# Kernel optimization log

Hardware: AMD Instinct MI355X
Metric: run time of the kernel (lower is better)

The kernel has to match this reference:

```python
import jax, jax.numpy as jnp
import numpy as np
from jax import lax


def _conv1d_t(x, w, pad):
    # x: [b, c, t], w: [o, c, k] -> [b, o, t]
    return lax.conv_general_dilated(x, w, (1,), ((pad, pad),),
                                    dimension_numbers=('NCH', 'OIH', 'NCH'))


def _ln_c(x, g, b, eps=1e-6):
    # LayerNorm over channel axis (axis=1) of [b, c, t] (channels_first)
    mu = x.mean(1, keepdims=True)
    var = ((x - mu) ** 2).mean(1, keepdims=True)
    return (x - mu) / jnp.sqrt(var + eps) * g[None, :, None] + b[None, :, None]


def _qgelu(x):
    return x * jax.nn.sigmoid(1.702 * x)


def _bn3d(x, g, b, eps=1e-5):
    # BatchNorm3d forward with batch statistics (training mode), x: [b, c, t, h, w]
    mu = x.mean((0, 2, 3, 4), keepdims=True)
    var = ((x - mu) ** 2).mean((0, 2, 3, 4), keepdims=True)
    return (x - mu) / jnp.sqrt(var + eps) * g[None, :, None, None, None] + b[None, :, None, None, None]


def setup_inputs() -> dict:
    key = jax.random.key(0)
    ks = jax.random.split(key, 8)
    B, C, T, H, Wd = 8, 256, 8, 56, 56
    CR = 64  # C // rf_r
    return {
        'feat': jax.random.normal(ks[0], (B, C, T, H, Wd), jnp.float32),
        'W': jax.random.normal(ks[1], (C, C, 3, 3), jnp.float32) * 0.02,
        'bias_p': jnp.zeros((C,), jnp.float32),
        'a_w': jax.random.normal(ks[2], (CR, C, 3), jnp.float32) * 0.02,
        'a_b': jnp.zeros((CR,), jnp.float32),
        'norm_w': jnp.ones((CR,), jnp.float32),
        'norm_b': jnp.zeros((CR,), jnp.float32),
        'normt_w': jnp.ones((CR,), jnp.float32),
        'normt_b': jnp.zeros((CR,), jnp.float32),
        'qkv_w': jax.random.normal(ks[3], (3 * CR, CR), jnp.float32) * 0.02,
        'qkv_b': jnp.zeros((3 * CR,), jnp.float32),
        'ao_w': jax.random.normal(ks[4], (CR, CR), jnp.float32) * 0.02,
        'ao_b': jnp.zeros((CR,), jnp.float32),
        'b_w': jax.random.normal(ks[5], (C, CR, 3), jnp.float32) * 0.02,
        'bb_w': jax.random.normal(ks[6], (C, CR, 3), jnp.float32) * 0.02,
        'gamma_a': jnp.ones((C,), jnp.float32),
        'beta_a': jnp.zeros((C,), jnp.float32),
        'gamma_b': jnp.zeros((C,), jnp.float32),
        'beta_b': jnp.zeros((C,), jnp.float32),
    }


HEAD_DIM = 64


def reference(feat, W, bias_p, a_w, a_b, norm_w, norm_b, normt_w, normt_b,
              qkv_w, qkv_b, ao_w, ao_b, b_w, bb_w,
              gamma_a, beta_a, gamma_b, beta_b):
    b, c_in, t, h, w = feat.shape
    c_out = W.shape[0]

    # ---- routing function (RouteFuncwTransformer) ----
    x = feat.mean((3, 4))                              # spatial avgpool -> [b, c, t]
    x = _conv1d_t(x, a_w, 1) + a_b[None, :, None]      # conv 'a' (kernel 3 over t)
    x = _ln_c(x, norm_w, norm_b)
    x = _qgelu(x)

    # temporal self-attention on 1x1-spatial tokens
    xn = _ln_c(x, normt_w, normt_b)
    c_r = xn.shape[1]
    nh = c_r // HEAD_DIM
    qkv = jnp.einsum('oc,bct->bot', qkv_w, xn) + qkv_b[None, :, None]
    qkv = qkv.reshape(b, 3, HEAD_DIM, nh, t)           # matches torch view(b,3,hd,nh,t)
    q = jnp.transpose(qkv[:, 0], (0, 2, 3, 1))         # [b, nh, t, hd]
    k = jnp.transpose(qkv[:, 1], (0, 2, 3, 1))
    v = jnp.transpose(qkv[:, 2], (0, 2, 3, 1))
    scale = c_r ** (-0.5)
    attn = jax.nn.softmax(jnp.einsum('bnqd,bnkd->bnqk', q, k) * scale, axis=-1)
    o = jnp.einsum('bnqk,bnkd->bnqd', attn, v)         # [b, nh, t, hd]
    o = jnp.transpose(o, (0, 1, 3, 2)).reshape(b, c_r, t)
    o = jnp.einsum('oc,bct->bot', ao_w, o) + ao_b[None, :, None]
    x = x + o

    w_alpha = _conv1d_t(x, b_w, 1)                     # [b, c_in, t] (zero_init_cal=False: no +1)
    b_alpha = _conv1d_t(x, bb_w, 1)                    # [b, c_out, t]

    # ---- calibrated conv; cin calibration == scaling input channels per (b,t) ----
    xs = (feat * w_alpha[:, :, :, None, None])
    xs = xs.transpose(0, 2, 1, 3, 4).reshape(b * t, c_in, h, w)
    out = lax.conv_general_dilated(xs, W, (1, 1), ((1, 1), (1, 1)),
                                   dimension_numbers=('NCHW', 'OIHW', 'NCHW'))
    bias_bt = b_alpha.transpose(0, 2, 1).reshape(b * t, c_out) * bias_p[None, :]
    out = out + bias_bt[:, :, None, None]
    out = out.reshape(b, t, c_out, h, w).transpose(0, 2, 1, 3, 4)  # [b, c_out, t, h, w]

    # ---- temporal aggregation: bn_a(out) + bn_b(avgpool_t3(out)) ----
    xp = jnp.pad(out, ((0, 0), (0, 0), (1, 1), (0, 0), (0, 0)))
    ap = (xp[:, :, :-2] + xp[:, :, 1:-1] + xp[:, :, 2:]) / 3.0
    return _bn3d(out, gamma_a, beta_a) + _bn3d(ap, gamma_b, beta_b)
```

## Files before the change

kernel.cpp:

```cpp
#include <hip/hip_runtime.h>
#include <hip/hip_bf16.h>

typedef __attribute__((ext_vector_type(8))) short short8;
typedef __attribute__((ext_vector_type(4))) float f32x4;

#define CI_STRIDE 25088

__device__ inline unsigned pk2_bf16(float a, float b){
  union {float f; unsigned u;} x, y;
  x.f = a; y.f = b;
  unsigned xa = x.u + 0x7fffu + ((x.u >> 16) & 1u);
  unsigned yb = y.u + 0x7fffu + ((y.u >> 16) & 1u);
  return (xa >> 16) | (yb & 0xffff0000u);
}

__global__ __launch_bounds__(256) void k_prep(const float* __restrict__ W,
                                              short* __restrict__ Wb,
                                              float* __restrict__ stats){
  if (blockIdx.x == 0){
    #pragma unroll
    for (int k = 0; k < 4; ++k) stats[threadIdx.x*4 + k] = 0.f;
  }
  int idx = blockIdx.x*256 + threadIdx.x;
  int kxy = idx >> 16;
  int r = idx & 65535;
  int co = r >> 8, ci = r & 255;
  float v = W[(size_t)(co*256 + ci)*9 + kxy];
  union {float f; unsigned u;} uu; uu.f = v;
  unsigned q = uu.u + 0x7fffu + ((uu.u >> 16) & 1u);
  Wb[idx] = (short)(q >> 16);
}

__global__ __launch_bounds__(256) void k_mean(const float* __restrict__ feat,
                                              float* __restrict__ x0){
  int id = blockIdx.x;
  const f32x4* src = (const f32x4*)(feat + (size_t)id*3136);
  float s = 0.f;
  for (int i = threadIdx.x; i < 784; i += 256){
    f32x4 v = src[i];
    s += (v.x + v.y) + (v.z + v.w);
  }
  for (int o = 32; o; o >>= 1) s += __shfl_down(s, o, 64);
  __shared__ float wsum[4];
  int lane = threadIdx.x & 63, w = threadIdx.x >> 6;
  if (!lane) wsum[w] = s;
  __syncthreads();
  if (threadIdx.x == 0) x0[id] = (wsum[0]+wsum[1]+wsum[2]+wsum[3]) * (1.f/3136.f);
}

__global__ __launch_bounds__(256) void k_route(
    const float* __restrict__ x0, const float* __restrict__ a_w, const float* __restrict__ a_b,
    const float* __restrict__ norm_w, const float* __restrict__ norm_b,
    const float* __restrict__ normt_w, const float* __restrict__ normt_b,
    const float* __restrict__ qkv_w, const float* __restrict__ qkv_b,
    const float* __restrict__ ao_w, const float* __restrict__ ao_b,
    const float* __restrict__ b_w, const float* __restrict__ bb_w,
    const float* __restrict__ bias_p,
    float* __restrict__ wa, float* __restrict__ bbt){
  __shared__ float x0l[2048];
  __shared__ float x1[512];
  __shared__ float x2[512];
  __shared__ float xn[512];
  __shared__ float qkvl[1536];
  __shared__ float att[64];
  __shared__ float ol[512];
  __shared__ float x3[512];
  __shared__ float mu8[8], rs8[8];
  int b = blockIdx.x, tid = threadIdx.x;

  for (int i = tid; i < 2048; i += 256) x0l[i] = x0[b*2048 + i];
  __syncthreads();

  for (int o = tid; o < 512; o += 256){
    int cr = o >> 3, t = o & 7;
    float acc = a_b[cr];
    const float* aw = a_w + cr*768;
    const float* xc = x0l + t;
    for (int c = 0; c < 256; ++c){
      float s = aw[c*3+1] * xc[c*8];
      if (t > 0) s += aw[c*3]   * xc[c*8 - 1];
      if (t < 7) s += aw[c*3+2] * xc[c*8 + 1];
      acc += s;
    }
    x1[o] = acc;
  }
  __syncthreads();

  if (tid < 8){
    float s = 0.f, q = 0.f;
    for (int cr = 0; cr < 64; ++cr){ float v = x1[cr*8 + tid]; s += v; q += v*v; }
    float mu = s * (1.f/64.f);
    float var = q * (1.f/64.f) - mu*mu;
    mu8[tid] = mu; rs8[tid] = rsqrtf(var + 1e-6f);
  }
  __syncthreads();
  for (int o = tid; o < 512; o += 256){
    int cr = o >> 3, t = o & 7;
    float v = (x1[o] - mu8[t]) * rs8[t] * norm_w[cr] + norm_b[cr];
    x2[o] = v * (1.f / (1.f + __expf(-1.702f * v)));
  }
  __syncthreads();

  if (tid < 8){
    float s = 0.f, q = 0.f;
    for (int cr = 0; cr < 64; ++cr){ float v = x2[cr*8 + tid]; s += v; q += v*v; }
    float mu = s * (1.f/64.f);
    float var = q * (1.f/64.f) - mu*mu;
    mu8[tid] = mu; rs8[tid] = rsqrtf(var + 1e-6f);
  }
  __syncthreads();
  for (int o = tid; o < 512; o += 256){
    int cr = o >> 3, t = o & 7;
    xn[o] = (x2[o] - mu8[t]) * rs8[t] * normt_w[cr] + normt_b[cr];
  }
  __syncthreads();

  for (int o = tid; o < 1536; o += 256){
    int oc = o >> 3, t = o & 7;
    float acc = qkv_b[oc];
    const float* qw = qkv_w + oc*64;
    for (int c = 0; c < 64; ++c) acc += qw[c] * xn[c*8 + t];
    qkvl[o] = acc;
  }
  __syncthreads();

  if (tid < 64){
    int tq = tid >> 3, tk = tid & 7;
    float s = 0.f;
    for (int d = 0; d < 64; ++d) s += qkvl[d*8 + tq] * qkvl[(64+d)*8 + tk];
    att[tid] = s * 0.125f;
  }
  __syncthreads();
  if (tid < 8){
    float m = att[tid*8];
    for (int k = 1; k < 8; ++k) m = fmaxf(m, att[tid*8 + k]);
    float e[8]; float s = 0.f;
    for (int k = 0; k < 8; ++k){ e[k] = __expf(att[tid*8 + k] - m); s += e[k]; }
    float inv = 1.f / s;
    for (int k = 0; k < 8; ++k) att[tid*8 + k] = e[k] * inv;
  }
  __syncthreads();
  for (int o = tid; o < 512; o += 256){
    int tq = o >> 6, d = o & 63;
    float acc = 0.f;
    for (int k = 0; k < 8; ++k) acc += att[tq*8 + k] * qkvl[(128+d)*8 + k];
    ol[o] = acc;
  }
  __syncthreads();
  for (int o = tid; o < 512; o += 256){
    int cr = o >> 3, t = o & 7;
    float acc = ao_b[cr];
    const float* aw = ao_w + cr*64;
    for (int d = 0; d < 64; ++d) acc += aw[d] * ol[t*64 + d];
    x3[o] = x2[o] + acc;
  }
  __syncthreads();
  for (int o = tid; o < 2048; o += 256){
    int c = o >> 3, t = o & 7;
    float wacc = 0.f, bacc = 0.f;
    const float* xc = x3 + t;
    const float* bw  = b_w  + c*192;
    const float* bw2 = bb_w + c*192;
    for (int cr = 0; cr < 64; ++cr){
      float xm = xc[cr*8];
      wacc += bw[cr*3+1]*xm;  bacc += bw2[cr*3+1]*xm;
      if (t > 0){ float xl = xc[cr*8-1]; wacc += bw[cr*3]*xl;   bacc += bw2[cr*3]*xl; }
      if (t < 7){ float xr = xc[cr*8+1]; wacc += bw[cr*3+2]*xr; bacc += bw2[cr*3+2]*xr; }
    }
    wa[b*2048 + o] = wacc;
    bbt[(b*8 + t)*256 + c] = bacc * bias_p[c];
  }
}

__global__ __launch_bounds__(256) void k_conv(const float* __restrict__ feat,
                                              const short* __restrict__ Wb,
                                              const float* __restrict__ wa,
                                              const float* __restrict__ bbt,
                                              float* __restrict__ out){
  __shared__ short buf[2][58*256];
  __shared__ float wal[256];

  int bid = blockIdx.x;
  int swz = (bid & 7)*448 + (bid >> 3);
  int img = swz / 56, y = swz - img*56;
  int b = img >> 3, t = img & 7;
  int tid = threadIdx.x;
  int lane = tid & 63, wave = tid >> 6;
  int arow = lane & 15, agrp = lane >> 4;

  wal[tid] = wa[(b*256 + tid)*8 + t];
  __syncthreads();

  const float* fb = feat + (size_t)b*256*8*3136 + (size_t)t*3136;

  f32x4 acc[4][4] = {};

  auto stage = [&](int bi, int ky){
    short* dst = buf[bi];
    int yin = y + ky - 1;
    bool rowok = (yin >= 0) && (yin < 56);
    const float* rsrc = fb + (size_t)yin*56;
    for (int i = tid; i < 128*58; i += 256){
      int ci2 = i / 58;
      int col = i - ci2*58;
      int ci = ci2 << 1;
      float v0 = 0.f, v1 = 0.f;
      int x = col - 1;
      if (rowok && (unsigned)x < 56u){
        v0 = rsrc[(size_t)ci*CI_STRIDE + x]     * wal[ci];
        v1 = rsrc[(size_t)(ci+1)*CI_STRIDE + x] * wal[ci+1];
      }
      unsigned p = pk2_bf16(v0, v1);
      int addr = ((col << 9) | (ci << 1)) ^ ((col & 7) << 4);
      *(unsigned*)((char*)dst + addr) = p;
    }
  };

  auto compute = [&](int bi, int ky){
    const short* sbuf = buf[bi];
    for (int kx = 0; kx < 3; ++kx){
      const short* wsl = Wb + (size_t)(ky*3 + kx)*65536 + (wave*64 + arow)*256 + (agrp << 3);
      for (int cs = 0; cs < 8; ++cs){
        int ci0 = (cs << 5) + (agrp << 3);
        short8 af[4], bfr[4];
        #pragma unroll
        for (int cf = 0; cf < 4; ++cf)
          af[cf] = *(const short8*)(wsl + cf*16*256 + (cs << 5));
        #pragma unroll
        for (int pf = 0; pf < 4; ++pf){
          int col = (pf << 4) + arow + kx;
          if (col > 57) col = 57;
          int addr = ((col << 9) | (ci0 << 1)) ^ ((col & 7) << 4);
          bfr[pf] = *(const short8*)((const char*)sbuf + addr);
        }
        #pragma unroll
        for (int cf = 0; cf < 4; ++cf){
          #pragma unroll
          for (int pf = 0; pf < 4; ++pf)
            acc[cf][pf] = __builtin_amdgcn_mfma_f32_16x16x32_bf16(af[cf], bfr[pf], acc[cf][pf], 0, 0, 0);
        }
      }
    }
  };

  stage(0, 0);
  __syncthreads();
  stage(1, 1);
  compute(0, 0);
  __syncthreads();
  stage(0, 2);
  compute(1, 1);
  __syncthreads();
  compute(0, 2);

  float* obase = out + (size_t)b*256*8*3136 + (size_t)t*3136 + y*56;
  const float* bb = bbt + (b*8 + t)*256;
  #pragma unroll
  for (int cf = 0; cf < 4; ++cf){
    int co0 = wave*64 + cf*16 + agrp*4;
    #pragma unroll
    for (int r = 0; r < 4; ++r){
      int co = co0 + r;
      float bias = bb[co];
      float* orow = obase + (size_t)co*CI_STRIDE;
      #pragma unroll
      for (int pf = 0; pf < 4; ++pf){
        int x = (pf << 4) + arow;
        if (x < 56) orow[x] = acc[cf][pf][r] + bias;
      }
    }
  }
}

__global__ __launch_bounds__(256) void k_stats(const float* __restrict__ out,
                                               float* __restrict__ stats){
  int bc = blockIdx.x;
  int c = bc & 255;
  const f32x4* base = (const f32x4*)(out + (size_t)bc*CI_STRIDE);
  float so = 0.f, ss = 0.f, sp = 0.f, sq = 0.f;
  const float inv3 = 1.f/3.f;
  for (int i = threadIdx.x; i < 784; i += 256){
    f32x4 v[8];
    #pragma unroll
    for (int t2 = 0; t2 < 8; ++t2) v[t2] = base[t2*784 + i];
    #pragma unroll
    for (int t2 = 0; t2 < 8; ++t2){
      f32x4 x = v[t2];
      so += (x.x + x.y) + (x.z + x.w);
      ss += (x.x*x.x + x.y*x.y) + (x.z*x.z + x.w*x.w);
    }
    #pragma unroll
    for (int t2 = 0; t2 < 8; ++t2){
      f32x4 s = v[t2];
      if (t2 > 0) s = s + v[t2-1];
      if (t2 < 7) s = s + v[t2+1];
      f32x4 a = s * inv3;
      sp += (a.x + a.y) + (a.z + a.w);
      sq += (a.x*a.x + a.y*a.y) + (a.z*a.z + a.w*a.w);
    }
  }
  for (int o = 32; o; o >>= 1){
    so += __shfl_down(so, o, 64); ss += __shfl_down(ss, o, 64);
    sp += __shfl_down(sp, o, 64); sq += __shfl_down(sq, o, 64);
  }
  __shared__ float red[4][4];
  int lane = threadIdx.x & 63, w = threadIdx.x >> 6;
  if (!lane){ red[w][0] = so; red[w][1] = ss; red[w][2] = sp; red[w][3] = sq; }
  __syncthreads();
  if (threadIdx.x < 4){
    float s = red[0][threadIdx.x] + red[1][threadIdx.x] + red[2][threadIdx.x] + red[3][threadIdx.x];
    atomicAdd(&stats[c*4 + threadIdx.x], s);
  }
}

__global__ void k_scale(const float* __restrict__ stats,
                        const float* __restrict__ ga, const float* __restrict__ ba_,
                        const float* __restrict__ gb, const float* __restrict__ bb_,
                        float* __restrict__ scale){
  int c = threadIdx.x;
  const float n = 200704.f;
  float mu_a = stats[c*4]   / n;
  float va   = stats[c*4+1] / n - mu_a*mu_a;
  float mu_p = stats[c*4+2] / n;
  float vp   = stats[c*4+3] / n - mu_p*mu_p;
  float ra = rsqrtf(va + 1e-5f) * ga[c];
  float rp = rsqrtf(vp + 1e-5f) * gb[c];
  scale[c*3]   = ra;
  scale[c*3+1] = rp;
  scale[c*3+2] = ba_[c] + bb_[c] - mu_a*ra - mu_p*rp;
}

__global__ __launch_bounds__(256) void k_final(float* __restrict__ out,
                                               const float* __restrict__ scale){
  int bc = blockIdx.x;
  int c = bc & 255;
  float ra  = scale[c*3];
  float rp  = scale[c*3+1];
  float off = scale[c*3+2];
  f32x4* base = (f32x4*)(out + (size_t)bc*CI_STRIDE);
  const float inv3 = 1.f/3.f;
  for (int i = threadIdx.x; i < 784; i += 256){
    f32x4 v[8];
    #pragma unroll
    for (int t2 = 0; t2 < 8; ++t2) v[t2] = base[t2*784 + i];
    #pragma unroll
    for (int t2 = 0; t2 < 8; ++t2){
      f32x4 s = v[t2];
      if (t2 > 0) s = s + v[t2-1];
      if (t2 < 7) s = s + v[t2+1];
      f32x4 o = v[t2]*ra + (s*inv3)*rp + off;
      base[t2*784 + i] = o;
    }
  }
}

extern "C" void kernel_launch(void* const* d_in, const int* in_sizes, int n_in,
                              void* d_out, int out_size, void* d_ws, size_t ws_size,
                              hipStream_t stream){
  (void)in_sizes; (void)n_in; (void)out_size; (void)ws_size;
  const float* feat    = (const float*)d_in[0];
  const float* W       = (const float*)d_in[1];
  const float* bias_p  = (const float*)d_in[2];
  const float* a_w     = (const float*)d_in[3];
  const float* a_b     = (const float*)d_in[4];
  const float* norm_w  = (const float*)d_in[5];
  const float* norm_b  = (const float*)d_in[6];
  const float* normt_w = (const float*)d_in[7];
  const float* normt_b = (const float*)d_in[8];
  const float* qkv_w   = (const float*)d_in[9];
  const float* qkv_b   = (const float*)d_in[10];
  const float* ao_w    = (const float*)d_in[11];
  const float* ao_b    = (const float*)d_in[12];
  const float* b_w     = (const float*)d_in[13];
  const float* bb_w    = (const float*)d_in[14];
  const float* gamma_a = (const float*)d_in[15];
  const float* beta_a  = (const float*)d_in[16];
  const float* gamma_b = (const float*)d_in[17];
  const float* beta_b  = (const float*)d_in[18];
  float* out = (float*)d_out;

  char* ws = (char*)d_ws;
  short* Wb    = (short*)ws;
  float* x0    = (float*)(ws + 1179648);
  float* wa    = (float*)(ws + 1179648 + 65536);
  float* bbt   = (float*)(ws + 1179648 + 2*65536);
  float* stats = (float*)(ws + 1179648 + 3*65536);
  float* scale = (float*)(ws + 1179648 + 3*65536 + 4096);

  k_prep <<<2304, 256, 0, stream>>>(W, Wb, stats);
  k_mean <<<16384, 256, 0, stream>>>(feat, x0);
  k_route<<<8, 256, 0, stream>>>(x0, a_w, a_b, norm_w, norm_b, normt_w, normt_b,
                                 qkv_w, qkv_b, ao_w, ao_b, b_w, bb_w, bias_p, wa, bbt);
  k_conv <<<3584, 256, 0, stream>>>(feat, Wb, wa, bbt, out);
  k_stats<<<2048, 256, 0, stream>>>(out, stats);
  k_scale<<<1, 256, 0, stream>>>(stats, gamma_a, beta_a, gamma_b, beta_b, scale);
  k_final<<<2048, 256, 0, stream>>>(out, scale);
}
```

Before: 1.426 ms.

## Pre-materialize scaled bf16 padded input rows and stream them into LDS asynchronously

Adds a k_xs kernel that scales feat by the per-channel calibration, converts it to bf16, pads it and writes swizzled rows to a workspace buffer. The conv kernel then copies these rows into LDS with global_load_lds DMA instead of doing strided fp32 gathers and conversion inside the conv loop. This removes the per-block redundant conversion work (each input row was staged by three conv blocks) and the uncoalesced loads. In exchange it adds a ~110MB intermediate write and read plus an extra launch, and it falls back to the old kernel when the workspace is too small.

```diff
diff --git a/kernel.cpp b/kernel.cpp
--- a/kernel.cpp
+++ b/kernel.cpp
@@ -13,6 +13,10 @@
   unsigned yb = y.u + 0x7fffu + ((y.u >> 16) & 1u);
   return (xa >> 16) | (yb & 0xffff0000u);
 }
+
+#define GL2LDS16(g, l) __builtin_amdgcn_global_load_lds( \
+    (const __attribute__((address_space(1))) void*)(g),  \
+    (__attribute__((address_space(3))) void*)(l), 16, 0, 0)
 
 __global__ __launch_bounds__(256) void k_prep(const float* __restrict__ W,
                                               short* __restrict__ Wb,
@@ -172,13 +176,55 @@
   }
 }
 
-__global__ __launch_bounds__(256) void k_conv(const float* __restrict__ feat,
-                                              const short* __restrict__ Wb,
-                                              const float* __restrict__ wa,
-                                              const float* __restrict__ bbt,
-                                              float* __restrict__ out){
-  __shared__ short buf[2][58*256];
-  __shared__ float wal[256];
+__global__ __launch_bounds__(256) void k_xs(const float* __restrict__ feat,
+                                            const float* __restrict__ wa,
+                                            short* __restrict__ xs){
+  __shared__ short lbuf[14848];
+  int bid = blockIdx.x;
+  int img = bid / 58, r = bid - img*58;
+  int b = img >> 3, t = img & 7;
+  int tid = threadIdx.x;
+
+  f32x4* l4 = (f32x4*)lbuf;
+  for (int i = tid; i < 1856; i += 256) l4[i] = f32x4{0.f,0.f,0.f,0.f};
+  __syncthreads();
+
+  if (r > 0 && r < 57){
+    int y = r - 1;
+    int p = tid & 127, h = tid >> 7;
+    int ci = p*2;
+    float s0 = wa[(b*256 + ci)*8 + t];
+    float s1 = wa[(b*256 + ci + 1)*8 + t];
+    const float* f0 = feat + (size_t)b*2048*3136 + (size_t)ci*CI_STRIDE + t*3136 + y*56 + h*28;
+    const f32x4* F0 = (const f32x4*)f0;
+    const f32x4* F1 = (const f32x4*)(f0 + CI_STRIDE);
+    int c4off = (ci >> 6)*128;
+    int w2 = (ci & 63)*2;
+    #pragma unroll
+    for (int j4 = 0; j4 < 7; ++j4){
+      f32x4 a = F0[j4], c = F1[j4];
+      #pragma unroll
+      for (int e = 0; e < 4; ++e){
+        int x = h*28 + j4*4 + e;
+        int cc = x + 1;
+        unsigned pk = pk2_bf16(a[e]*s0, c[e]*s1);
+        int swz = ((2*r + cc) & 7) << 4;
+        int addr = cc*512 + c4off + (w2 ^ swz);
+        *(unsigned*)((char*)lbuf + addr) = pk;
+      }
+    }
+  }
+  __syncthreads();
+
+  f32x4* dst = (f32x4*)(xs + (size_t)(img*58 + r)*14848);
+  for (int i = tid; i < 1856; i += 256) dst[i] = l4[i];
+}
+
+__global__ __launch_bounds__(256) void k_conv2(const short* __restrict__ xs,
+                                               const short* __restrict__ Wb,
+                                               const float* __restrict__ bbt,
+                                               float* __restrict__ out){
+  __shared__ short buf[2][14848];
 
   int bid = blockIdx.x;
   int swz = (bid & 7)*448 + (bid >> 3);
@@ -188,11 +234,100 @@
   int lane = tid & 63, wave = tid >> 6;
   int arow = lane & 15, agrp = lane >> 4;
 
+  const short* src = xs + (size_t)img*58*14848;
+
+  f32x4 acc[4][4] = {};
+
+  auto stage = [&](int bi, int r){
+    const char* g = (const char*)(src + (size_t)r*14848);
+    char* l = (char*)&buf[bi][0];
+    int base = wave*464;
+    for (int j = lane; j < 464; j += 64){
+      int idx = base + j;
+      GL2LDS16(g + idx*16, l + idx*16);
+    }
+  };
+
+  auto compute = [&](int bi, int ky){
+    const short* sb = buf[bi];
+    int rr2 = (2*(y + ky)) & 7;
+    for (int kx = 0; kx < 3; ++kx){
+      const short* wsl = Wb + (size_t)(ky*3 + kx)*65536 + (wave*64 + arow)*256;
+      for (int cs = 0; cs < 8; ++cs){
+        short8 af[4], bfr[4];
+        #pragma unroll
+        for (int cf = 0; cf < 4; ++cf)
+          af[cf] = *(const short8*)(wsl + cf*4096 + cs*32 + agrp*8);
+        int c4 = (cs >> 1)*128;
+        int w2 = ((cs & 1) << 6) | (agrp << 4);
+        #pragma unroll
+        for (int pf = 0; pf < 4; ++pf){
+          int cc = (pf << 4) + arow + kx;
+          if (cc > 57) cc = 57;
+          int addr = cc*512 + c4 + (w2 ^ (((rr2 + cc) & 7) << 4));
+          bfr[pf] = *(const short8*)((const char*)sb + addr);
+        }
+        #pragma unroll
+        for (int cf = 0; cf < 4; ++cf){
+          #pragma unroll
+          for (int pf = 0; pf < 4; ++pf)
+            acc[cf][pf] = __builtin_amdgcn_mfma_f32_16x16x32_bf16(af[cf], bfr[pf], acc[cf][pf], 0, 0, 0);
+        }
+      }
+    }
+  };
+
+  stage(0, y);
+  stage(1, y + 1);
+  asm volatile("s_waitcnt vmcnt(0)" ::: "memory");
+  __builtin_amdgcn_s_barrier();
+  compute(0, 0);
+  __syncthreads();
+  stage(0, y + 2);
+  compute(1, 1);
+  asm volatile("s_waitcnt vmcnt(0)" ::: "memory");
+  __builtin_amdgcn_s_barrier();
+  compute(0, 2);
+
+  float* obase = out + (size_t)b*256*8*3136 + (size_t)t*3136 + y*56;
+  const float* bb = bbt + (b*8 + t)*256;
+  #pragma unroll
+  for (int cf = 0; cf < 4; ++cf){
+    int co0 = wave*64 + cf*16 + agrp*4;
+    #pragma unroll
+    for (int r = 0; r < 4; ++r){
+      int co = co0 + r;
+      float bias = bb[co];
+      float* orow = obase + (size_t)co*CI_STRIDE;
+      #pragma unroll
+      for (int pf = 0; pf < 4; ++pf){
+        int x = (pf << 4) + arow;
+        if (x < 56) orow[x] = acc[cf][pf][r] + bias;
+      }
+    }
+  }
+}
+
+__global__ __launch_bounds__(256) void k_conv_fb(const float* __restrict__ feat,
+                                                 const short* __restrict__ Wb,
+                                                 const float* __restrict__ wa,
+                                                 const float* __restrict__ bbt,
+                                                 float* __restrict__ out){
+  __shared__ short buf[2][58*256];
+  __shared__ float wal[256];
+
+  int bid = blockIdx.x;
+  int swz = (bid & 7)*448 + (bid >> 3);
+  int img = swz / 56, y = swz - img*56;
+  int b = img >> 3, t = img & 7;
+  int tid = threadIdx.x;
+  int lane = tid & 63, wave = tid >> 6;
+  int arow = lane & 15, agrp = lane >> 4;
+
   wal[tid] = wa[(b*256 + tid)*8 + t];
   __syncthreads();
 
   const float* fb = feat + (size_t)b*256*8*3136 + (size_t)t*3136;
-
   f32x4 acc[4][4] = {};
 
   auto stage = [&](int bi, int ky){
@@ -357,7 +492,7 @@
 extern "C" void kernel_launch(void* const* d_in, const int* in_sizes, int n_in,
                               void* d_out, int out_size, void* d_ws, size_t ws_size,
                               hipStream_t stream){
-  (void)in_sizes; (void)n_in; (void)out_size; (void)ws_size;
+  (void)in_sizes; (void)n_in; (void)out_size;
   const float* feat    = (const float*)d_in[0];
   const float* W       = (const float*)d_in[1];
   const float* bias_p  = (const float*)d_in[2];
@@ -386,12 +521,20 @@
   float* bbt   = (float*)(ws + 1179648 + 2*65536);
   float* stats = (float*)(ws + 1179648 + 3*65536);
   float* scale = (float*)(ws + 1179648 + 3*65536 + 4096);
+  short* xs    = (short*)(ws + 1383424);
+  const size_t NEED = 1383424ull + 110231552ull;
+  bool fast = ws_size >= NEED;
 
   k_prep <<<2304, 256, 0, stream>>>(W, Wb, stats);
   k_mean <<<16384, 256, 0, stream>>>(feat, x0);
   k_route<<<8, 256, 0, stream>>>(x0, a_w, a_b, norm_w, norm_b, normt_w, normt_b,
                                  qkv_w, qkv_b, ao_w, ao_b, b_w, bb_w, bias_p, wa, bbt);
-  k_conv <<<3584, 256, 0, stream>>>(feat, Wb, wa, bbt, out);
+  if (fast){
+    k_xs   <<<3712, 256, 0, stream>>>(feat, wa, xs);
+    k_conv2<<<3584, 256, 0, stream>>>(xs, Wb, bbt, out);
+  } else {
+    k_conv_fb<<<3584, 256, 0, stream>>>(feat, Wb, wa, bbt, out);
+  }
   k_stats<<<2048, 256, 0, stream>>>(out, stats);
   k_scale<<<1, 256, 0, stream>>>(stats, gamma_a, beta_a, gamma_b, beta_b, scale);
   k_final<<<2048, 256, 0, stream>>>(out, scale);
```

Result: faster. 1.271 ms (-10.8%).
